# Kernel tuning notes

Measured on AMD Instinct MI355X. Metric: run time of the kernel, lower is better.

## Reference

```python
import jax, jax.numpy as jnp
import numpy as np
from jax import lax

B = 64      # batch (n_image == n_caption)
R = 36      # image regions
W = 32      # words per caption (uniform cap_lens)
D = 1024    # embedding dim
LAMBDA_SOFTMAX = 9.0
LAMBDA_LSE = 6.0
ALPHA = 0.1
MARGIN = 0.2
OT_ITER = 20
BETA = 0.5
EPS = 1e-8


def setup_inputs() -> dict:
    key = jax.random.key(0)
    k1, k2, k3 = jax.random.split(key, 3)
    im = jax.random.normal(k1, (B, R, D), jnp.float32)
    s = jax.random.normal(k2, (B, W, D), jnp.float32)
    x = jax.random.normal(k3, (B, W, D), jnp.float32)
    s_l = jnp.full((B,), W, dtype=jnp.int32)
    return {"im": im, "s": s, "s_l": s_l, "x": x}


def _l2norm(a, axis):
    # matches torch l2norm: x / (sqrt(sum(x^2)) + eps)
    return a / (jnp.sqrt(jnp.sum(a * a, axis=axis, keepdims=True)) + EPS)


def _scores_t2i(im, s, x):
    # ---- func_attention (t2i): query = caption words, context = image regions ----
    # raw attn: (c, i, r, w) = context @ query^T for every caption/image pair
    attn = jnp.einsum('ird,cwd->cirw', im, s)
    attn = jax.nn.leaky_relu(attn, negative_slope=0.1)   # clipped_l2norm
    attn = _l2norm(attn, axis=3)                          # l2norm over query (word) axis
    attn = jnp.swapaxes(attn, 2, 3)                       # (c, i, w, r)
    attn = jax.nn.softmax(attn * LAMBDA_SOFTMAX, axis=3)  # softmax over regions
    wctx = jnp.einsum('ciwr,ird->ciwd', attn, im)         # weighted context (c,i,w,d)

    # cosine similarity between caption words and weighted context, over d
    num = jnp.einsum('cwd,ciwd->ciw', s, wctx)
    w1 = jnp.linalg.norm(s, axis=2)[:, None, :]           # (c,1,w)
    w2 = jnp.linalg.norm(wctx, axis=3)                    # (c,i,w)
    row_sim = num / jnp.maximum(w1 * w2, EPS)             # (c,i,w)

    # LogSumExp aggregation over words
    sim = jax.nn.logsumexp(row_sim * LAMBDA_LSE, axis=2) / LAMBDA_LSE  # (c,i)

    # ---- OT cost matrix: cosine distance between x words and image regions ----
    xn = x / (jnp.linalg.norm(x, axis=2, keepdims=True) + 1e-12)
    imn = im / (jnp.linalg.norm(im, axis=2, keepdims=True) + 1e-12)
    C = 1.0 - jnp.einsum('cwd,ird->ciwr', xn, imn)        # (c,i,W,R)

    # ---- IPOT (uniform marginals, beta=0.5, one inner step) ----
    A = jnp.exp(-C / BETA)
    T0 = jnp.ones_like(C)
    sigma0 = jnp.full(C.shape[:2] + (R,), 1.0 / R, dtype=C.dtype)

    def body(carry, _):
        T, sigma = carry
        Q = A * T                                          # (c,i,W,R)
        delta = 1.0 / (W * jnp.einsum('ciwr,cir->ciw', Q, sigma))
        sigma = 1.0 / (R * jnp.einsum('ciwr,ciw->cir', Q, delta))
        T = delta[..., :, None] * Q * sigma[..., None, :]
        return (T, sigma), None

    (T, _), _ = lax.scan(body, (T0, sigma0), None, length=OT_ITER)
    ot_dist = jnp.sum(C * T, axis=(-2, -1))               # trace(C^T T) -> (c,i)
    ot_sim = -ot_dist

    # torch code concatenates per-caption columns: scores[img, cap]
    return sim.T, ot_sim.T                                 # (n_img, n_cap)


def reference(im, s, s_l, x):
    # s_l is uniform (== W); the per-caption slicing in the torch loop is a no-op.
    scores, scores_ot = _scores_t2i(im, s, x)
    n = scores.shape[0]

    diag = jnp.diagonal(scores)
    diag_ot = jnp.diagonal(scores_ot)

    cost_s = jnp.maximum(MARGIN + scores - diag[:, None], 0.0)
    cost_im = jnp.maximum(MARGIN + scores - diag[None, :], 0.0)
    cost_s_ot = jnp.maximum(MARGIN + scores_ot - diag_ot[:, None], 0.0)
    cost_im_ot = jnp.maximum(MARGIN + scores_ot - diag_ot[None, :], 0.0)

    off = 1.0 - jnp.eye(n, dtype=scores.dtype)
    cost_s = cost_s * off
    cost_im = cost_im * off
    cost_s_ot = cost_s_ot * off
    cost_im_ot = cost_im_ot * off

    cost_s = cost_s + ALPHA * cost_s_ot
    cost_im = cost_im + ALPHA * cost_im_ot

    # max_violation = True
    cost_s = jnp.max(cost_s, axis=1)
    cost_im = jnp.max(cost_im, axis=0)
    cost_s_ot = jnp.max(cost_s_ot, axis=1)
    cost_im_ot = jnp.max(cost_im_ot, axis=0)

    return (jnp.sum(cost_s) + jnp.sum(cost_im),
            jnp.sum(cost_s_ot) + jnp.sum(cost_im_ot))
```

## Files before the change

kernel.cpp:

```cpp
#include <hip/hip_runtime.h>
#include <cstdint>
#include <cstddef>


typedef __attribute__((ext_vector_type(8))) short short8;
typedef __attribute__((ext_vector_type(4))) float f32x4;
typedef __attribute__((ext_vector_type(2))) float f2;

__device__ __forceinline__ unsigned short f2bf(float f) {
  unsigned u = __float_as_uint(f);
  u += 0x7FFFu + ((u >> 16) & 1u);
  return (unsigned short)(u >> 16);
}
__device__ __forceinline__ float rcpf(float x) { return __builtin_amdgcn_rcpf(x); }

__global__ __launch_bounds__(256) void k_prep(const float* __restrict__ s,
                                              const float* __restrict__ x,
                                              const float* __restrict__ im,
                                              unsigned short* __restrict__ Ab,
                                              unsigned short* __restrict__ Bb,
                                              float* __restrict__ w1,
                                              float* __restrict__ xn_r,
                                              float* __restrict__ imn_r,
                                              float* __restrict__ G) {
  int blk = blockIdx.x;
  if (blk < 2304) {
    int b = blk / 36, r = blk - b * 36;
    int wid = threadIdx.x >> 6, l = threadIdx.x & 63;
    const float* rowr = im + ((size_t)b*36 + r) * 1024;
    float4 my[4];
    #pragma unroll
    for (int j = 0; j < 4; ++j) my[j] = ((const float4*)rowr)[j*64 + l];
    float* Gr = G + ((size_t)b*36 + r) * 36;
    for (int rp = wid; rp < 36; rp += 4) {
      const float* rowp = im + ((size_t)b*36 + rp) * 1024;
      float p = 0.f;
      #pragma unroll
      for (int j = 0; j < 4; ++j) {
        float4 u = ((const float4*)rowp)[j*64 + l];
        p += my[j].x*u.x + my[j].y*u.y + my[j].z*u.z + my[j].w*u.w;
      }
      #pragma unroll
      for (int o = 32; o > 0; o >>= 1) p += __shfl_down(p, o, 64);
      if (l == 0) Gr[rp] = p;
    }
    return;
  }
  int row = blk - 2304, tid = threadIdx.x;
  const float* src; unsigned short* dst; float* np; int recip;
  if (row < 2048)      { src = s  + (size_t)row * 1024;          dst = Ab + (size_t)row * 1024;          np = w1    + row;          recip = 0; }
  else if (row < 4096) { src = x  + (size_t)(row - 2048) * 1024; dst = Ab + (size_t)row * 1024;          np = xn_r  + (row - 2048); recip = 1; }
  else                 { src = im + (size_t)(row - 4096) * 1024; dst = Bb + (size_t)(row - 4096) * 1024; np = imn_r + (row - 4096); recip = 1; }
  float4 f = ((const float4*)src)[tid];
  ushort4 h;
  h.x = f2bf(f.x); h.y = f2bf(f.y); h.z = f2bf(f.z); h.w = f2bf(f.w);
  ((ushort4*)dst)[tid] = h;
  float p = f.x*f.x + f.y*f.y + f.z*f.z + f.w*f.w;
  #pragma unroll
  for (int o = 32; o > 0; o >>= 1) p += __shfl_down(p, o, 64);
  __shared__ float red[4];
  if ((tid & 63) == 0) red[tid >> 6] = p;
  __syncthreads();
  if (tid == 0) {
    float n = sqrtf(red[0] + red[1] + red[2] + red[3]);
    *np = recip ? 1.f / (n + 1e-12f) : n;
  }
}

__global__ __launch_bounds__(256) void k_gemm_mfma(const unsigned short* __restrict__ A,
                                                   const unsigned short* __restrict__ B,
                                                   unsigned short* __restrict__ dot) {
  __shared__ unsigned short lA[128 * 32];
  __shared__ unsigned short lB[96 * 32];
  int tid = threadIdx.x;
  int bn = blockIdx.x * 96, bm = blockIdx.y * 128;
  int wid = tid >> 6, l = tid & 63;
  int wr = (wid >> 1) * 64, wc = (wid & 1) * 48;
  int lr = l & 15, lq = l >> 4;

  f32x4 acc[4][3] = {};

  int row_a = tid >> 2;
  int kq = (tid & 3) * 8;
  const unsigned short* gA = A + (size_t)(bm + row_a) * 1024 + kq;
  const unsigned short* gB = B + (size_t)(bn + row_a) * 1024 + kq;
  unsigned loff = (unsigned)tid * 16u;

  for (int kt = 0; kt < 1024; kt += 32) {
    __builtin_amdgcn_global_load_lds(
        (const __attribute__((address_space(1))) void*)(gA + kt),
        (__attribute__((address_space(3))) void*)((char*)lA + loff), 16, 0, 0);
    __builtin_amdgcn_global_load_lds(
        (const __attribute__((address_space(1))) void*)(gA + 64*1024 + kt),
        (__attribute__((address_space(3))) void*)((char*)lA + 4096 + loff), 16, 0, 0);
    __builtin_amdgcn_global_load_lds(
        (const __attribute__((address_space(1))) void*)(gB + kt),
        (__attribute__((address_space(3))) void*)((char*)lB + loff), 16, 0, 0);
    if (tid < 128)
      __builtin_amdgcn_global_load_lds(
          (const __attribute__((address_space(1))) void*)(gB + 64*1024 + kt),
          (__attribute__((address_space(3))) void*)((char*)lB + 4096 + loff), 16, 0, 0);
    __syncthreads();

    short8 af[4], bfr[3];
    #pragma unroll
    for (int mi = 0; mi < 4; ++mi)
      af[mi] = *(const short8*)&lA[(wr + mi*16 + lr) * 32 + lq * 8];
    #pragma unroll
    for (int ni = 0; ni < 3; ++ni)
      bfr[ni] = *(const short8*)&lB[(wc + ni*16 + lr) * 32 + lq * 8];
    #pragma unroll
    for (int mi = 0; mi < 4; ++mi)
      #pragma unroll
      for (int ni = 0; ni < 3; ++ni)
        acc[mi][ni] = __builtin_amdgcn_mfma_f32_16x16x32_bf16(af[mi], bfr[ni], acc[mi][ni], 0, 0, 0);
    __syncthreads();
  }

  #pragma unroll
  for (int mi = 0; mi < 4; ++mi)
    #pragma unroll
    for (int ni = 0; ni < 3; ++ni) {
      int gcol = bn + wc + ni*16 + lr;
      #pragma unroll
      for (int q = 0; q < 4; ++q) {
        int grow = bm + wr + mi*16 + lq*4 + q;
        dot[(size_t)grow * 2304 + gcol] = f2bf(acc[mi][ni][q]);
      }
    }
}

template<int C>
__device__ __forceinline__ float dpp_add(float v) {
  return v + __int_as_float(__builtin_amdgcn_mov_dpp(__float_as_int(v), C, 0xF, 0xF, true));
}
template<int C>
__device__ __forceinline__ float dpp_max(float v) {
  return fmaxf(v, __int_as_float(__builtin_amdgcn_mov_dpp(__float_as_int(v), C, 0xF, 0xF, true)));
}
__device__ __forceinline__ float bsum32(float v) {
  v = dpp_add<0xB1>(v);
  v = dpp_add<0x4E>(v);
  v = dpp_add<0x141>(v);
  v = dpp_add<0x128>(v);
  v += __shfl_xor(v, 16, 64);
  return v;
}
__device__ __forceinline__ float bmax32(float v) {
  v = dpp_max<0xB1>(v);
  v = dpp_max<0x4E>(v);
  v = dpp_max<0x141>(v);
  v = dpp_max<0x128>(v);
  v = fmaxf(v, __shfl_xor(v, 16, 64));
  return v;
}

__global__ __launch_bounds__(256, 3) void k_pair(const unsigned short* __restrict__ dotb,
                                                 const float* __restrict__ Gm,
                                                 const float* __restrict__ w1m,
                                                 const float* __restrict__ xnrm,
                                                 const float* __restrict__ imnrm,
                                                 float* __restrict__ S,
                                                 float* __restrict__ Sot) {
  int wid  = threadIdx.x >> 6;
  int pair = blockIdx.x * 4 + wid;
  int c = pair >> 6, i = pair & 63;
  int l = threadIdx.x & 63;
  int h = l >> 5, w = l & 31;
  int r0 = h * 18;

  const unsigned* drow = (const unsigned*)(dotb + (size_t)(c*32 + w) * 2304 + i*36 + r0);
  const unsigned* xrow = (const unsigned*)((const unsigned short*)drow + (size_t)2048 * 2304);
  float w1  = w1m[c*32 + w];
  float xnr = xnrm[c*32 + w];

  f2 d2[9], Cm2[9];
  #pragma unroll
  for (int k = 0; k < 9; ++k) {
    unsigned u = drow[k];
    d2[k][0] = __uint_as_float(u << 16);
    d2[k][1] = __uint_as_float(u & 0xFFFF0000u);
  }
  const f2* ir = (const f2*)(imnrm + i*36 + r0);
  #pragma unroll
  for (int k = 0; k < 9; ++k) {
    unsigned u = xrow[k];
    f2 xv;
    xv[0] = __uint_as_float(u << 16);
    xv[1] = __uint_as_float(u & 0xFFFF0000u);
    xv *= xnr;
    Cm2[k] = 1.f - xv * ir[k];
  }

  f2 f[9];
  #pragma unroll
  for (int k = 0; k < 9; ++k) {
    f2 t = d2[k] * 0.1f;
    f[k][0] = fmaxf(d2[k][0], t[0]);
    f[k][1] = fmaxf(d2[k][1], t[1]);
  }
  f2 p2[9];
  #pragma unroll
  for (int k = 0; k < 9; ++k) {
    f2 sq = f[k] * f[k];
    float t0 = bsum32(sq[0]);
    float t1 = bsum32(sq[1]);
    f2 rs;
    rs[0] = __builtin_amdgcn_rsqf(fmaxf(t0 * 0.012345679f, 1e-30f));
    rs[1] = __builtin_amdgcn_rsqf(fmaxf(t1 * 0.012345679f, 1e-30f));
    p2[k] = f[k] * rs;
  }
  float mx = fmaxf(fmaxf(p2[0][0], p2[0][1]), fmaxf(p2[1][0], p2[1][1]));
  #pragma unroll
  for (int k = 2; k < 9; ++k) mx = fmaxf(mx, fmaxf(p2[k][0], p2[k][1]));
  mx = fmaxf(mx, __shfl_xor(mx, 32, 64));

  f2 e2[9];
  f2 sum2 = {0.f, 0.f}, nu2 = {0.f, 0.f};
  #pragma unroll
  for (int k = 0; k < 9; ++k) {
    e2[k][0] = __expf(p2[k][0] - mx);
    e2[k][1] = __expf(p2[k][1] - mx);
    sum2 += e2[k];
    nu2 += e2[k] * d2[k];
  }
  float sum = sum2[0] + sum2[1];
  float numu = nu2[0] + nu2[1];
  sum  += __shfl_xor(sum, 32, 64);
  numu += __shfl_xor(numu, 32, 64);
  float inv = rcpf(sum);
  float num = numu * inv;

  f2 afull[18];
  #pragma unroll
  for (int k = 0; k < 9; ++k) {
    f2 a = e2[k] * inv;
    f2 o;
    o[0] = __shfl_xor(a[0], 32, 64);
    o[1] = __shfl_xor(a[1], 32, 64);
    afull[k][0]     = h ? o[0] : a[0];
    afull[k][1]     = h ? o[1] : a[1];
    afull[9 + k][0] = h ? a[0] : o[0];
    afull[9 + k][1] = h ? a[1] : o[1];
  }

  int iu = __builtin_amdgcn_readfirstlane(i);
  const float* Gi = Gm + (size_t)iu * 1296;
  float w2sq = 0.f;
  #pragma unroll 4
  for (int rp = 0; rp < 36; ++rp) {
    const f2* Gr = (const f2*)(Gi + rp * 36);
    f2 in2 = {0.f, 0.f};
    #pragma unroll
    for (int q = 0; q < 18; ++q) in2 += Gr[q] * afull[q];
    float ar = (rp & 1) ? afull[rp >> 1][1] : afull[rp >> 1][0];
    w2sq = fmaf(ar, in2[0] + in2[1], w2sq);
  }
  float w2 = __builtin_amdgcn_sqrtf(w2sq);
  float rs6 = 6.f * num * rcpf(fmaxf(w1 * w2, 1e-8f));

  float mw = bmax32(rs6);
  float se = bsum32(__expf(rs6 - mw));
  float sim = (mw + __logf(se)) * (1.f / 6.f);
  if (l == 0) S[i*64 + c] = sim;

  f2 Am2[9], Qm2[9], sg2[9];
  #pragma unroll
  for (int k = 0; k < 9; ++k) {
    Am2[k][0] = __expf(-2.f * Cm2[k][0]);
    Am2[k][1] = __expf(-2.f * Cm2[k][1]);
    Qm2[k] = Am2[k];
    sg2[k] = (f2){1.f/36.f, 1.f/36.f};
  }
  float delta = 0.f;
  for (int it = 0; it < 20; ++it) {
    f2 t2 = {0.f, 0.f};
    #pragma unroll
    for (int k = 0; k < 9; ++k) t2 += Qm2[k] * sg2[k];
    float tt = t2[0] + t2[1];
    tt += __shfl_xor(tt, 32, 64);
    delta = rcpf(32.f * tt);
    #pragma unroll
    for (int k = 0; k < 9; ++k) {
      f2 qd = Qm2[k] * delta;
      float q0 = bsum32(qd[0]);
      float q1 = bsum32(qd[1]);
      sg2[k][0] = rcpf(36.f * q0);
      sg2[k][1] = rcpf(36.f * q1);
    }
    if (it < 19) {
      #pragma unroll
      for (int k = 0; k < 9; ++k) Qm2[k] = (Am2[k] * delta) * Qm2[k] * sg2[k];
    }
  }
  f2 ot2 = {0.f, 0.f};
  #pragma unroll
  for (int k = 0; k < 9; ++k) ot2 += Cm2[k] * (Qm2[k] * delta * sg2[k]);
  float ot = ot2[0] + ot2[1];
  ot += __shfl_xor(ot, 32, 64);
  ot = bsum32(ot);
  if (l == 0) Sot[i*64 + c] = -ot;
}

__global__ __launch_bounds__(256) void k_reduce(const float* __restrict__ Sg,
                                                const float* __restrict__ Sotg,
                                                float* __restrict__ outp) {
  __shared__ float s[4096];
  __shared__ float so[4096];
  __shared__ float red0[256], red1[256];
  int tid = threadIdx.x;
  for (int e = tid; e < 4096; e += 256) { s[e] = Sg[e]; so[e] = Sotg[e]; }
  __syncthreads();
  float m0 = 0.f, m1 = 0.f;
  if (tid < 64) {
    int i = tid;
    float di = s[i*65], dio = so[i*65];
    for (int c2 = 0; c2 < 64; ++c2) {
      if (c2 == i) continue;
      float cs  = fmaxf(0.2f + s[i*64 + c2]  - di,  0.f);
      float cso = fmaxf(0.2f + so[i*64 + c2] - dio, 0.f);
      m0 = fmaxf(m0, cs + 0.1f * cso);
      m1 = fmaxf(m1, cso);
    }
  } else if (tid < 128) {
    int c2 = tid - 64;
    float dc = s[c2*65], dco = so[c2*65];
    for (int i = 0; i < 64; ++i) {
      if (i == c2) continue;
      float cim  = fmaxf(0.2f + s[i*64 + c2]  - dc,  0.f);
      float cimo = fmaxf(0.2f + so[i*64 + c2] - dco, 0.f);
      m0 = fmaxf(m0, cim + 0.1f * cimo);
      m1 = fmaxf(m1, cimo);
    }
  }
  red0[tid] = m0; red1[tid] = m1;
  __syncthreads();
  if (tid == 0) {
    float a0 = 0.f, a1 = 0.f;
    for (int t = 0; t < 128; ++t) { a0 += red0[t]; a1 += red1[t]; }
    outp[0] = a0;
    outp[1] = a1;
  }
}

extern "C" void kernel_launch(void* const* d_in, const int* in_sizes, int n_in,
                              void* d_out, int out_size, void* d_ws, size_t ws_size,
                              hipStream_t stream) {
  (void)in_sizes; (void)n_in; (void)out_size; (void)ws_size;
  const float* im = (const float*)d_in[0];
  const float* s  = (const float*)d_in[1];
  const float* x  = (const float*)d_in[3];
  float* out = (float*)d_out;

  unsigned short* Ab   = (unsigned short*)d_ws;
  unsigned short* Bb   = Ab + (size_t)4096 * 1024;
  unsigned short* dotb = Bb + (size_t)2304 * 1024;
  float* G     = (float*)(dotb + (size_t)4096 * 2304);
  float* w1    = G + 64*36*36;
  float* xn_r  = w1 + 2048;
  float* imn_r = xn_r + 2048;
  float* S     = imn_r + 2304;
  float* Sot   = S + 4096;

  k_prep<<<dim3(8704), 256, 0, stream>>>(s, x, im, Ab, Bb, w1, xn_r, imn_r, G);
  k_gemm_mfma<<<dim3(24, 32), 256, 0, stream>>>(Ab, Bb, dotb);
  k_pair<<<dim3(1024), 256, 0, stream>>>(dotb, G, w1, xn_r, imn_r, S, Sot);
  k_reduce<<<dim3(1), 256, 0, stream>>>(S, Sot, out);
}
```

Baseline: 114.8 us.

## Fuse GEMM into per-pair kernel computing dot tiles with direct-load MFMA

```diff
diff --git a/kernel.cpp b/kernel.cpp
--- a/kernel.cpp
+++ b/kernel.cpp
@@ -67,69 +67,6 @@
   }
 }
 
-__global__ __launch_bounds__(256) void k_gemm_mfma(const unsigned short* __restrict__ A,
-                                                   const unsigned short* __restrict__ B,
-                                                   unsigned short* __restrict__ dot) {
-  __shared__ unsigned short lA[128 * 32];
-  __shared__ unsigned short lB[96 * 32];
-  int tid = threadIdx.x;
-  int bn = blockIdx.x * 96, bm = blockIdx.y * 128;
-  int wid = tid >> 6, l = tid & 63;
-  int wr = (wid >> 1) * 64, wc = (wid & 1) * 48;
-  int lr = l & 15, lq = l >> 4;
-
-  f32x4 acc[4][3] = {};
-
-  int row_a = tid >> 2;
-  int kq = (tid & 3) * 8;
-  const unsigned short* gA = A + (size_t)(bm + row_a) * 1024 + kq;
-  const unsigned short* gB = B + (size_t)(bn + row_a) * 1024 + kq;
-  unsigned loff = (unsigned)tid * 16u;
-
-  for (int kt = 0; kt < 1024; kt += 32) {
-    __builtin_amdgcn_global_load_lds(
-        (const __attribute__((address_space(1))) void*)(gA + kt),
-        (__attribute__((address_space(3))) void*)((char*)lA + loff), 16, 0, 0);
-    __builtin_amdgcn_global_load_lds(
-        (const __attribute__((address_space(1))) void*)(gA + 64*1024 + kt),
-        (__attribute__((address_space(3))) void*)((char*)lA + 4096 + loff), 16, 0, 0);
-    __builtin_amdgcn_global_load_lds(
-        (const __attribute__((address_space(1))) void*)(gB + kt),
-        (__attribute__((address_space(3))) void*)((char*)lB + loff), 16, 0, 0);
-    if (tid < 128)
-      __builtin_amdgcn_global_load_lds(
-          (const __attribute__((address_space(1))) void*)(gB + 64*1024 + kt),
-          (__attribute__((address_space(3))) void*)((char*)lB + 4096 + loff), 16, 0, 0);
-    __syncthreads();
-
-    short8 af[4], bfr[3];
-    #pragma unroll
-    for (int mi = 0; mi < 4; ++mi)
-      af[mi] = *(const short8*)&lA[(wr + mi*16 + lr) * 32 + lq * 8];
-    #pragma unroll
-    for (int ni = 0; ni < 3; ++ni)
-      bfr[ni] = *(const short8*)&lB[(wc + ni*16 + lr) * 32 + lq * 8];
-    #pragma unroll
-    for (int mi = 0; mi < 4; ++mi)
-      #pragma unroll
-      for (int ni = 0; ni < 3; ++ni)
-        acc[mi][ni] = __builtin_amdgcn_mfma_f32_16x16x32_bf16(af[mi], bfr[ni], acc[mi][ni], 0, 0, 0);
-    __syncthreads();
-  }
-
-  #pragma unroll
-  for (int mi = 0; mi < 4; ++mi)
-    #pragma unroll
-    for (int ni = 0; ni < 3; ++ni) {
-      int gcol = bn + wc + ni*16 + lr;
-      #pragma unroll
-      for (int q = 0; q < 4; ++q) {
-        int grow = bm + wr + mi*16 + lq*4 + q;
-        dot[(size_t)grow * 2304 + gcol] = f2bf(acc[mi][ni][q]);
-      }
-    }
-}
-
 template<int C>
 __device__ __forceinline__ float dpp_add(float v) {
   return v + __int_as_float(__builtin_amdgcn_mov_dpp(__float_as_int(v), C, 0xF, 0xF, true));
@@ -155,42 +92,86 @@
   return v;
 }
 
-__global__ __launch_bounds__(256, 3) void k_pair(const unsigned short* __restrict__ dotb,
-                                                 const float* __restrict__ Gm,
-                                                 const float* __restrict__ w1m,
-                                                 const float* __restrict__ xnrm,
-                                                 const float* __restrict__ imnrm,
-                                                 float* __restrict__ S,
-                                                 float* __restrict__ Sot) {
-  int wid  = threadIdx.x >> 6;
-  int pair = blockIdx.x * 4 + wid;
+__global__ __launch_bounds__(256, 4) void k_fused(const unsigned short* __restrict__ Ab,
+                                                  const unsigned short* __restrict__ Bb,
+                                                  const float* __restrict__ Gm,
+                                                  const float* __restrict__ w1m,
+                                                  const float* __restrict__ xnrm,
+                                                  const float* __restrict__ imnrm,
+                                                  float* __restrict__ S,
+                                                  float* __restrict__ Sot) {
+  __shared__ float lbuf[4][32 * 42];
+  int bid = (int)blockIdx.x;
+  int blk = (bid & 7) * 128 + (bid >> 3);
+  int wid = threadIdx.x >> 6;
+  int pair = blk * 4 + wid;
   int c = pair >> 6, i = pair & 63;
   int l = threadIdx.x & 63;
+  int lr = l & 15, lq = l >> 4;
+
+  const unsigned short* sA = Ab + (size_t)(c*32 + lr) * 1024 + lq*8;
+  const unsigned short* xA = sA + (size_t)2048 * 1024;
+  const unsigned short* iB = Bb + (size_t)(i*36 + lr) * 1024 + lq*8;
+  f32x4 sacc[2][3] = {};
+  f32x4 xacc[2][3] = {};
+  for (int kt = 0; kt < 1024; kt += 32) {
+    short8 a0 = *(const short8*)(sA + kt);
+    short8 a1 = *(const short8*)(sA + 16*1024 + kt);
+    short8 x0 = *(const short8*)(xA + kt);
+    short8 x1 = *(const short8*)(xA + 16*1024 + kt);
+    short8 b0 = *(const short8*)(iB + kt);
+    short8 b1 = *(const short8*)(iB + 16*1024 + kt);
+    short8 b2 = *(const short8*)(iB + 32*1024 + kt);
+    sacc[0][0] = __builtin_amdgcn_mfma_f32_16x16x32_bf16(a0, b0, sacc[0][0], 0, 0, 0);
+    sacc[0][1] = __builtin_amdgcn_mfma_f32_16x16x32_bf16(a0, b1, sacc[0][1], 0, 0, 0);
+    sacc[0][2] = __builtin_amdgcn_mfma_f32_16x16x32_bf16(a0, b2, sacc[0][2], 0, 0, 0);
+    sacc[1][0] = __builtin_amdgcn_mfma_f32_16x16x32_bf16(a1, b0, sacc[1][0], 0, 0, 0);
+    sacc[1][1] = __builtin_amdgcn_mfma_f32_16x16x32_bf16(a1, b1, sacc[1][1], 0, 0, 0);
+    sacc[1][2] = __builtin_amdgcn_mfma_f32_16x16x32_bf16(a1, b2, sacc[1][2], 0, 0, 0);
+    xacc[0][0] = __builtin_amdgcn_mfma_f32_16x16x32_bf16(x0, b0, xacc[0][0], 0, 0, 0);
+    xacc[0][1] = __builtin_amdgcn_mfma_f32_16x16x32_bf16(x0, b1, xacc[0][1], 0, 0, 0);
+    xacc[0][2] = __builtin_amdgcn_mfma_f32_16x16x32_bf16(x0, b2, xacc[0][2], 0, 0, 0);
+    xacc[1][0] = __builtin_amdgcn_mfma_f32_16x16x32_bf16(x1, b0, xacc[1][0], 0, 0, 0);
+    xacc[1][1] = __builtin_amdgcn_mfma_f32_16x16x32_bf16(x1, b1, xacc[1][1], 0, 0, 0);
+    xacc[1][2] = __builtin_amdgcn_mfma_f32_16x16x32_bf16(x1, b2, xacc[1][2], 0, 0, 0);
+  }
+
+  float* buf = lbuf[wid];
+  #pragma unroll
+  for (int mi = 0; mi < 2; ++mi)
+    #pragma unroll
+    for (int ni = 0; ni < 3; ++ni) {
+      int col = ni*16 + lr;
+      if (ni < 2 || lr < 4) {
+        #pragma unroll
+        for (int q = 0; q < 4; ++q)
+          buf[(mi*16 + lq*4 + q)*42 + col] = sacc[mi][ni][q];
+      }
+    }
+  asm volatile("s_waitcnt lgkmcnt(0)" ::: "memory");
+
   int h = l >> 5, w = l & 31;
   int r0 = h * 18;
-
-  const unsigned* drow = (const unsigned*)(dotb + (size_t)(c*32 + w) * 2304 + i*36 + r0);
-  const unsigned* xrow = (const unsigned*)((const unsigned short*)drow + (size_t)2048 * 2304);
+  const float* rowp = &buf[w*42 + r0];
+  f2 d2[9];
+  #pragma unroll
+  for (int k = 0; k < 9; ++k) d2[k] = *(const f2*)(rowp + 2*k);
+  asm volatile("s_waitcnt lgkmcnt(0)" ::: "memory");
+
+  #pragma unroll
+  for (int mi = 0; mi < 2; ++mi)
+    #pragma unroll
+    for (int ni = 0; ni < 3; ++ni) {
+      int col = ni*16 + lr;
+      if (ni < 2 || lr < 4) {
+        #pragma unroll
+        for (int q = 0; q < 4; ++q)
+          buf[(mi*16 + lq*4 + q)*42 + col] = xacc[mi][ni][q];
+      }
+    }
+
   float w1  = w1m[c*32 + w];
   float xnr = xnrm[c*32 + w];
-
-  f2 d2[9], Cm2[9];
-  #pragma unroll
-  for (int k = 0; k < 9; ++k) {
-    unsigned u = drow[k];
-    d2[k][0] = __uint_as_float(u << 16);
-    d2[k][1] = __uint_as_float(u & 0xFFFF0000u);
-  }
-  const f2* ir = (const f2*)(imnrm + i*36 + r0);
-  #pragma unroll
-  for (int k = 0; k < 9; ++k) {
-    unsigned u = xrow[k];
-    f2 xv;
-    xv[0] = __uint_as_float(u << 16);
-    xv[1] = __uint_as_float(u & 0xFFFF0000u);
-    xv *= xnr;
-    Cm2[k] = 1.f - xv * ir[k];
-  }
 
   f2 f[9];
   #pragma unroll
@@ -263,6 +244,18 @@
   float se = bsum32(__expf(rs6 - mw));
   float sim = (mw + __logf(se)) * (1.f / 6.f);
   if (l == 0) S[i*64 + c] = sim;
+
+  asm volatile("s_waitcnt lgkmcnt(0)" ::: "memory");
+  f2 Cm2[9];
+  {
+    const f2* ir = (const f2*)(imnrm + i*36 + r0);
+    #pragma unroll
+    for (int k = 0; k < 9; ++k) {
+      f2 xv = *(const f2*)(rowp + 2*k);
+      xv *= xnr;
+      Cm2[k] = 1.f - xv * ir[k];
+    }
+  }
 
   f2 Am2[9], Qm2[9], sg2[9];
   #pragma unroll
@@ -363,7 +356,6 @@
   float* Sot   = S + 4096;
 
   k_prep<<<dim3(8704), 256, 0, stream>>>(s, x, im, Ab, Bb, w1, xn_r, imn_r, G);
-  k_gemm_mfma<<<dim3(24, 32), 256, 0, stream>>>(Ab, Bb, dotb);
-  k_pair<<<dim3(1024), 256, 0, stream>>>(dotb, G, w1, xn_r, imn_r, S, Sot);
+  k_fused<<<dim3(1024), 256, 0, stream>>>(Ab, Bb, G, w1, xn_r, imn_r, S, Sot);
   k_reduce<<<dim3(1), 256, 0, stream>>>(S, Sot, out);
 }
```

Result: slower. 179.2 us (+56.1%).
